# Optimization experiments

Measured on AMD Instinct MI355X. Metric: run time of the kernel, lower is better.

## Reference

```python
import jax, jax.numpy as jnp
import numpy as np


def setup_inputs() -> dict:
    key = jax.random.key(0)
    k1, k2, k3, k4, k5 = jax.random.split(key, 5)
    B, C, H, W = 8, 512, 128, 128
    C2 = 128  # key_dim
    x = jax.random.normal(k1, (B, C, H, W), dtype=jnp.float32)
    # 1x1 conv weights stored as [out_ch, in_ch] (kernel is 1x1)
    wq = jax.random.normal(k2, (C2, C), dtype=jnp.float32) * (1.0 / np.sqrt(C))
    bq = jax.random.normal(k3, (C2,), dtype=jnp.float32) * 0.01
    wk = jax.random.normal(k4, (C2, C), dtype=jnp.float32) * (1.0 / np.sqrt(C))
    bk = jax.random.normal(k5, (C2,), dtype=jnp.float32) * 0.01
    return {"x": x, "wq": wq, "bq": bq, "wk": wk, "bk": bk}


def reference(x, wq, bq, wk, bk):
    # x: [B, C, H, W]
    # 1x1 conv projections (query_conv / key_conv)
    q = jnp.einsum('bchw,kc->bkhw', x, wq) + bq[None, :, None, None]  # [B,C2,H,W]
    k = jnp.einsum('bchw,kc->bkhw', x, wk) + bk[None, :, None, None]  # [B,C2,H,W]

    # --- attention along H axis (batched over W) ---
    # query_h = key.permute(0,3,2,1): [B,W,H,C2]; key_h = query.permute(0,3,1,2): [B,W,C2,H]
    energy_h = jnp.einsum('bwhc,bcgw->bwhg', jnp.transpose(k, (0, 3, 2, 1)), q)  # [B,W,H,H]
    attn_h = jax.nn.softmax(energy_h, axis=-1)
    # value_h = x.permute(0,3,2,1): [B,W,H,C]; out: [B,W,H,C] -> permute(0,3,2,1) -> [B,C,H,W]
    out_h = jnp.einsum('bwhg,bcgw->bchw', attn_h, x)

    # --- attention along W axis (batched over H) ---
    # query_w = key.permute(0,2,3,1): [B,H,W,C2]; key_w = query.permute(0,2,1,3): [B,H,C2,W]
    energy_w = jnp.einsum('bhwc,bchv->bhwv', jnp.transpose(k, (0, 2, 3, 1)), q)  # [B,H,W,W]
    attn_w = jax.nn.softmax(energy_w, axis=-1)
    # value_w = x.permute(0,2,3,1): [B,H,W,C]; out: [B,H,W,C] -> permute(0,3,1,2) -> [B,C,H,W]
    out_w = jnp.einsum('bhwv,bchv->bchw', attn_w, x)

    return out_h + out_w
```

## Files before the change

kernel.cpp:

```cpp
#include <hip/hip_runtime.h>
#include <hip/hip_fp16.h>

#define NB 8
#define NC 512
#define NK 128
#define NP 128
#define NHW 16384

typedef unsigned short u16;
typedef unsigned int u32;
typedef float f32x4 __attribute__((ext_vector_type(4)));
typedef _Float16 f16x8 __attribute__((ext_vector_type(8)));

__device__ __forceinline__ u16 f2h(float f) { return __half_as_ushort(__float2half(f)); }
__device__ __forceinline__ float h2f(u16 u) { return __half2float(__ushort_as_half(u)); }

__global__ __launch_bounds__(256) void wconv_kernel(const float* __restrict__ wq,
                                                    const float* __restrict__ wk,
                                                    u16* __restrict__ wh) {
    int row = blockIdx.x;
    const float* src = (row < 128) ? (wq + (size_t)row * NC) : (wk + (size_t)(row - 128) * NC);
    int t = threadIdx.x;
    float2 v = *(const float2*)(src + t * 2);
    ushort2 o; o.x = f2h(v.x); o.y = f2h(v.y);
    *(ushort2*)(wh + (size_t)row * NC + t * 2) = o;
}

__global__ __launch_bounds__(256) void convtr_kernel(const float* __restrict__ x,
                                                     u16* __restrict__ xt) {
    __shared__ u16 ts[32][36];
    int plane = blockIdx.y;
    int tile  = blockIdx.x;
    int h0 = (tile >> 2) * 32, w0 = (tile & 3) * 32;
    const float* ip = x + (size_t)plane * NHW;
    u16* op = xt + (size_t)plane * NHW;
    int r  = threadIdx.x >> 3;
    int c4 = (threadIdx.x & 7) * 4;
    float4 v = *(const float4*)(ip + (h0 + r) * NP + w0 + c4);
    ts[r][c4 + 0] = f2h(v.x); ts[r][c4 + 1] = f2h(v.y);
    ts[r][c4 + 2] = f2h(v.z); ts[r][c4 + 3] = f2h(v.w);
    __syncthreads();
    ushort4 o;
    o.x = ts[c4 + 0][r]; o.y = ts[c4 + 1][r]; o.z = ts[c4 + 2][r]; o.w = ts[c4 + 3][r];
    *(ushort4*)(op + (w0 + r) * NP + h0 + c4) = o;
}

#define XROW 40
__device__ __forceinline__ int xt2_off(int p, int cw) {
    int sw = ((p >> 3) & 3) << 2;
    return p * XROW + 2 * (cw ^ sw);
}

__global__ __launch_bounds__(256, 3) void proj_kernel(const float* __restrict__ x,
                                                      const u16* __restrict__ wh,
                                                      const float* __restrict__ bq,
                                                      const float* __restrict__ bk,
                                                      u16* __restrict__ q,
                                                      u16* __restrict__ k) {
    __shared__ __align__(16) u16 smem[9216];
    int b  = blockIdx.y;
    int p0 = blockIdx.x * 64;
    int tid = threadIdx.x;
    int lane = tid & 63, w = tid >> 6;
    int ln = lane & 15, g = lane >> 4;

    float biasv[4];
#pragma unroll
    for (int nf = 0; nf < 4; nf++) {
        int oc = w * 64 + nf * 16 + ln;
        biasv[nf] = (oc < 128) ? bq[oc] : bk[oc - 128];
    }

    f32x4 acc[4][4];
#pragma unroll
    for (int mf = 0; mf < 4; mf++)
#pragma unroll
        for (int nf = 0; nf < 4; nf++) acc[mf][nf] = 0.0f;

    int si  = tid >> 4;
    int spx = (tid & 15) * 4;

#define STAGE(buf, c0)                                                                  \
    {                                                                                   \
        const float* xa = x + ((size_t)(b * NC + (c0) + 2 * si)) * NHW + p0 + spx;      \
        const float* xb = xa + NHW;                                                     \
        float4 a0 = *(const float4*)xa;                                                 \
        float4 b0 = *(const float4*)xb;                                                 \
        float av[4] = {a0.x, a0.y, a0.z, a0.w};                                         \
        float bv[4] = {b0.x, b0.y, b0.z, b0.w};                                         \
        _Pragma("unroll") for (int j = 0; j < 4; j++) {                                 \
            ushort2 pk;                                                                 \
            pk.x = f2h(av[j]); pk.y = f2h(bv[j]);                                       \
            *(ushort2*)&smem[(buf) * 2560 + xt2_off(spx + j, si)] = pk;                 \
        }                                                                               \
    }

    STAGE(0, 0);
    __syncthreads();
    for (int t = 0; t < 16; ++t) {
        int c0 = t * 32;
        if (t < 15) STAGE((t + 1) & 1, c0 + 32);
        f16x8 bf[4];
#pragma unroll
        for (int nf = 0; nf < 4; nf++)
            bf[nf] = *(const f16x8*)&wh[((size_t)(w * 64 + nf * 16 + ln)) * NC + c0 + g * 8];
        f16x8 af[4];
#pragma unroll
        for (int mf = 0; mf < 4; mf++)
            af[mf] = *(const f16x8*)&smem[(t & 1) * 2560 + xt2_off(mf * 16 + ln, g * 4)];
#pragma unroll
        for (int mf = 0; mf < 4; mf++)
#pragma unroll
            for (int nf = 0; nf < 4; nf++)
                acc[mf][nf] = __builtin_amdgcn_mfma_f32_16x16x32_f16(af[mf], bf[nf], acc[mf][nf], 0, 0, 0);
        __syncthreads();
    }
#undef STAGE

#pragma unroll
    for (int pass = 0; pass < 2; pass++) {
        if ((w >> 1) == pass) {
            int colbase = (w & 1) * 64;
#pragma unroll
            for (int mf = 0; mf < 4; mf++)
#pragma unroll
                for (int nf = 0; nf < 4; nf++)
#pragma unroll
                    for (int rg = 0; rg < 4; rg++) {
                        int p = mf * 16 + g * 4 + rg;
                        smem[p * 136 + colbase + nf * 16 + ln] = f2h(acc[mf][nf][rg] + biasv[nf]);
                    }
        }
        __syncthreads();
        {
            int p = tid >> 2, seg = tid & 3;
            u16* dst = (pass == 0 ? q : k) + ((size_t)(b * NHW + p0 + p)) * NK + seg * 32;
            const u16* srcl = &smem[p * 136 + seg * 32];
            *(uint4*)(dst)     = *(const uint4*)(srcl);
            *(uint4*)(dst + 8) = *(const uint4*)(srcl + 8);
            *(uint4*)(dst + 16) = *(const uint4*)(srcl + 16);
            *(uint4*)(dst + 24) = *(const uint4*)(srcl + 24);
        }
        __syncthreads();
    }
}

template <int TR>
__global__ __launch_bounds__(256) void attn_kernel(const u16* __restrict__ q,
                                                   const u16* __restrict__ k,
                                                   const void* __restrict__ vsrc,
                                                   void* __restrict__ osrc) {
    __shared__ __align__(16) u16 smem[2 * 128 * 136];
    __shared__ float redmax[256];
    __shared__ float redsum[256];
    u16* Ks = smem;
    u16* Qs = smem + 128 * 136;
    u16* Al = smem;
    u16* Vl = smem + 128 * 136;

    int r = blockIdx.x, b = blockIdx.y;
    int tid = threadIdx.x;
    int lane = tid & 63, w = tid >> 6;
    int ln = lane & 15, g = lane >> 4;

    const size_t base = TR ? ((size_t)b * NHW + r) * NK : ((size_t)b * NHW + (size_t)r * NP) * NK;
    const int qrs = TR ? NP * NK : NK;

    {
        int j = tid >> 1, hf = tid & 1;
        const u16* qp2 = q + base + (size_t)j * qrs + hf * 64;
        const u16* kp2 = k + base + (size_t)j * qrs + hf * 64;
#pragma unroll
        for (int e = 0; e < 8; e++) {
            *(uint4*)&Qs[j * 136 + hf * 64 + e * 8] = *(const uint4*)(qp2 + e * 8);
            *(uint4*)&Ks[j * 136 + hf * 64 + e * 8] = *(const uint4*)(kp2 + e * 8);
        }
    }
    __syncthreads();

    int wj = w >> 1, wi = w & 1;
    f32x4 e[4][4];
#pragma unroll
    for (int mf = 0; mf < 4; mf++)
#pragma unroll
        for (int nf = 0; nf < 4; nf++) e[mf][nf] = 0.0f;
#pragma unroll
    for (int ks = 0; ks < 4; ks++) {
        f16x8 qa[4], kb[4];
#pragma unroll
        for (int mf = 0; mf < 4; mf++)
            qa[mf] = *(const f16x8*)&Qs[(wj * 64 + mf * 16 + ln) * 136 + ks * 32 + g * 8];
#pragma unroll
        for (int nf = 0; nf < 4; nf++)
            kb[nf] = *(const f16x8*)&Ks[(wi * 64 + nf * 16 + ln) * 136 + ks * 32 + g * 8];
#pragma unroll
        for (int mf = 0; mf < 4; mf++)
#pragma unroll
            for (int nf = 0; nf < 4; nf++)
                e[mf][nf] = __builtin_amdgcn_mfma_f32_16x16x32_f16(qa[mf], kb[nf], e[mf][nf], 0, 0, 0);
    }

    float pm[4];
#pragma unroll
    for (int nf = 0; nf < 4; nf++) {
        pm[nf] = -3.0e38f;
#pragma unroll
        for (int mf = 0; mf < 4; mf++)
#pragma unroll
            for (int rg = 0; rg < 4; rg++) pm[nf] = fmaxf(pm[nf], e[mf][nf][rg]);
        pm[nf] = fmaxf(pm[nf], __shfl_xor(pm[nf], 16));
        pm[nf] = fmaxf(pm[nf], __shfl_xor(pm[nf], 32));
    }
    if (g == 0) {
#pragma unroll
        for (int nf = 0; nf < 4; nf++) redmax[wj * 128 + wi * 64 + nf * 16 + ln] = pm[nf];
    }
    __syncthreads();
    float fm[4];
#pragma unroll
    for (int nf = 0; nf < 4; nf++) {
        int i = wi * 64 + nf * 16 + ln;
        fm[nf] = fmaxf(redmax[i], redmax[128 + i]);
    }
    float ps[4] = {0.f, 0.f, 0.f, 0.f};
#pragma unroll
    for (int mf = 0; mf < 4; mf++)
#pragma unroll
        for (int nf = 0; nf < 4; nf++)
#pragma unroll
            for (int rg = 0; rg < 4; rg++) {
                float v = __expf(e[mf][nf][rg] - fm[nf]);
                e[mf][nf][rg] = v;
                ps[nf] += v;
            }
#pragma unroll
    for (int nf = 0; nf < 4; nf++) {
        ps[nf] += __shfl_xor(ps[nf], 16);
        ps[nf] += __shfl_xor(ps[nf], 32);
    }
    if (g == 0) {
#pragma unroll
        for (int nf = 0; nf < 4; nf++) redsum[wj * 128 + wi * 64 + nf * 16 + ln] = ps[nf];
    }
    __syncthreads();
    float ivs[4];
#pragma unroll
    for (int nf = 0; nf < 4; nf++) {
        int i = wi * 64 + nf * 16 + ln;
        ivs[nf] = 1.0f / (redsum[i] + redsum[128 + i]);
    }
#pragma unroll
    for (int mf = 0; mf < 4; mf++)
#pragma unroll
        for (int nf = 0; nf < 4; nf++) {
            ushort4 pk;
            pk.x = f2h(e[mf][nf][0] * ivs[nf]);
            pk.y = f2h(e[mf][nf][1] * ivs[nf]);
            pk.z = f2h(e[mf][nf][2] * ivs[nf]);
            pk.w = f2h(e[mf][nf][3] * ivs[nf]);
            *(ushort4*)&Al[(wi * 64 + nf * 16 + ln) * 136 + wj * 64 + mf * 16 + g * 4] = pk;
        }
    __syncthreads();

    int wc = w >> 1, wi2 = w & 1;
    f16x8 bfr[4][4];
#pragma unroll
    for (int nf2 = 0; nf2 < 4; nf2++)
#pragma unroll
        for (int js = 0; js < 4; js++)
            bfr[nf2][js] = *(const f16x8*)&Al[(wi2 * 64 + nf2 * 16 + ln) * 136 + js * 32 + g * 8];

    for (int c0 = 0; c0 < NC; c0 += 64) {
        {
            int cc = tid >> 2, ch = (tid & 3) * 32;
            if (TR == 0) {
                const float* vp = (const float*)vsrc + ((size_t)(b * NC + c0 + cc)) * NHW + (size_t)r * NP + ch;
                u16 tmp[32];
#pragma unroll
                for (int q4 = 0; q4 < 8; q4++) {
                    float4 vv = *(const float4*)(vp + q4 * 4);
                    tmp[q4 * 4 + 0] = f2h(vv.x);
                    tmp[q4 * 4 + 1] = f2h(vv.y);
                    tmp[q4 * 4 + 2] = f2h(vv.z);
                    tmp[q4 * 4 + 3] = f2h(vv.w);
                }
#pragma unroll
                for (int q8 = 0; q8 < 4; q8++)
                    *(uint4*)&Vl[cc * 136 + ch + q8 * 8] = *(uint4*)&tmp[q8 * 8];
            } else {
                const u16* vp = (const u16*)vsrc + ((size_t)(b * NC + c0 + cc)) * NHW + (size_t)r * NP + ch;
#pragma unroll
                for (int q8 = 0; q8 < 4; q8++)
                    *(uint4*)&Vl[cc * 136 + ch + q8 * 8] = *(const uint4*)(vp + q8 * 8);
            }
        }
        __syncthreads();
        f32x4 o[2][4];
#pragma unroll
        for (int mf2 = 0; mf2 < 2; mf2++)
#pragma unroll
            for (int nf2 = 0; nf2 < 4; nf2++) o[mf2][nf2] = 0.0f;
#pragma unroll
        for (int js = 0; js < 4; js++) {
            f16x8 va[2];
#pragma unroll
            for (int mf2 = 0; mf2 < 2; mf2++)
                va[mf2] = *(const f16x8*)&Vl[(wc * 32 + mf2 * 16 + ln) * 136 + js * 32 + g * 8];
#pragma unroll
            for (int mf2 = 0; mf2 < 2; mf2++)
#pragma unroll
                for (int nf2 = 0; nf2 < 4; nf2++)
                    o[mf2][nf2] = __builtin_amdgcn_mfma_f32_16x16x32_f16(va[mf2], bfr[nf2][js], o[mf2][nf2], 0, 0, 0);
        }
#pragma unroll
        for (int mf2 = 0; mf2 < 2; mf2++)
#pragma unroll
            for (int nf2 = 0; nf2 < 4; nf2++)
#pragma unroll
                for (int rg = 0; rg < 4; rg++) {
                    int ci = c0 + wc * 32 + mf2 * 16 + g * 4 + rg;
                    int ii = wi2 * 64 + nf2 * 16 + ln;
                    size_t oa = ((size_t)(b * NC + ci)) * NHW + (size_t)r * NP + ii;
                    if (TR == 0) ((float*)osrc)[oa] = o[mf2][nf2][rg];
                    else         ((u16*)osrc)[oa] = f2h(o[mf2][nf2][rg]);
                }
        __syncthreads();
    }
}

__global__ __launch_bounds__(256) void addtr_kernel(const u16* __restrict__ oht,
                                                    float* __restrict__ out) {
    __shared__ u16 ts[32][36];
    int plane = blockIdx.y;
    int tile  = blockIdx.x;
    int h0 = (tile >> 2) * 32, w0 = (tile & 3) * 32;
    int r  = threadIdx.x >> 3;
    int c4 = (threadIdx.x & 7) * 4;
    ushort4 v = *(const ushort4*)(oht + (size_t)plane * NHW + (w0 + r) * NP + h0 + c4);
    ts[r][c4 + 0] = v.x; ts[r][c4 + 1] = v.y; ts[r][c4 + 2] = v.z; ts[r][c4 + 3] = v.w;
    __syncthreads();
    float* dst = out + (size_t)plane * NHW + (h0 + r) * NP + w0 + c4;
    float4 cur = *(const float4*)dst;
    cur.x += h2f(ts[c4 + 0][r]);
    cur.y += h2f(ts[c4 + 1][r]);
    cur.z += h2f(ts[c4 + 2][r]);
    cur.w += h2f(ts[c4 + 3][r]);
    *(float4*)dst = cur;
}

extern "C" void kernel_launch(void* const* d_in, const int* in_sizes, int n_in,
                              void* d_out, int out_size, void* d_ws, size_t ws_size,
                              hipStream_t stream) {
    const float* x  = (const float*)d_in[0];
    const float* wq = (const float*)d_in[1];
    const float* bq = (const float*)d_in[2];
    const float* wk = (const float*)d_in[3];
    const float* bk = (const float*)d_in[4];
    float* out = (float*)d_out;

    const size_t QKE = (size_t)NB * NHW * NK;
    const size_t XE  = (size_t)NB * NC * NHW;
    u16* q   = (u16*)d_ws;
    u16* k   = q + QKE;
    u16* xt  = k + QKE;
    u16* oht = xt + XE;
    u16* wh  = oht + XE;

    dim3 blk(256);

    wconv_kernel<<<dim3(256), blk, 0, stream>>>(wq, wk, wh);
    convtr_kernel<<<dim3(16, NB * NC), blk, 0, stream>>>(x, xt);
    proj_kernel<<<dim3(NHW / 64, NB), blk, 0, stream>>>(x, wh, bq, bk, q, k);
    attn_kernel<1><<<dim3(NP, NB), blk, 0, stream>>>(q, k, (const void*)xt, (void*)oht);
    attn_kernel<0><<<dim3(NP, NB), blk, 0, stream>>>(q, k, (const void*)x, (void*)out);
    addtr_kernel<<<dim3(16, NB * NC), blk, 0, stream>>>(oht, out);
}
```

Before: 505.2 us.

## Prefetch next V chunk into registers and store W-attention output as fp16

The attention kernel now loads the next 64-channel V slice into registers while MFMAs run on the current slice, overlapping global loads with compute. When the workspace is large enough, the W-axis attention writes fp16 output to a scratch buffer and a new combine kernel reads both fp16 partial outputs and writes the fp32 result. This avoids an fp32 write followed by a read-modify-write of the output. It adds register pressure from the prefetch buffer and lowers the precision of the W-branch output to fp16.

Result: faster. 494.8 us (-2.1%).

```diff
diff --git a/kernel.cpp b/kernel.cpp
--- a/kernel.cpp
+++ b/kernel.cpp
@@ -145,7 +145,7 @@
     }
 }
 
-template <int TR>
+template <int TR, int OH>
 __global__ __launch_bounds__(256) void attn_kernel(const u16* __restrict__ q,
                                                    const u16* __restrict__ k,
                                                    const void* __restrict__ vsrc,
@@ -270,31 +270,33 @@
         for (int js = 0; js < 4; js++)
             bfr[nf2][js] = *(const f16x8*)&Al[(wi2 * 64 + nf2 * 16 + ln) * 136 + js * 32 + g * 8];
 
+    int cc = tid >> 2, ch = (tid & 3) * 32;
+    u16 vh[32];
+#define LOADV(c0)                                                                           \
+    {                                                                                       \
+        if (TR == 0) {                                                                      \
+            const float* vn = (const float*)vsrc + ((size_t)(b * NC + (c0) + cc)) * NHW +   \
+                              (size_t)r * NP + ch;                                          \
+            _Pragma("unroll") for (int e2 = 0; e2 < 8; e2++) {                              \
+                float4 vv = *(const float4*)(vn + e2 * 4);                                  \
+                vh[e2 * 4 + 0] = f2h(vv.x); vh[e2 * 4 + 1] = f2h(vv.y);                     \
+                vh[e2 * 4 + 2] = f2h(vv.z); vh[e2 * 4 + 3] = f2h(vv.w);                     \
+            }                                                                               \
+        } else {                                                                            \
+            const u16* vn = (const u16*)vsrc + ((size_t)(b * NC + (c0) + cc)) * NHW +       \
+                            (size_t)r * NP + ch;                                            \
+            _Pragma("unroll") for (int e2 = 0; e2 < 4; e2++)                                \
+                *(uint4*)&vh[e2 * 8] = *(const uint4*)(vn + e2 * 8);                        \
+        }                                                                                   \
+    }
+
+    LOADV(0);
     for (int c0 = 0; c0 < NC; c0 += 64) {
-        {
-            int cc = tid >> 2, ch = (tid & 3) * 32;
-            if (TR == 0) {
-                const float* vp = (const float*)vsrc + ((size_t)(b * NC + c0 + cc)) * NHW + (size_t)r * NP + ch;
-                u16 tmp[32];
-#pragma unroll
-                for (int q4 = 0; q4 < 8; q4++) {
-                    float4 vv = *(const float4*)(vp + q4 * 4);
-                    tmp[q4 * 4 + 0] = f2h(vv.x);
-                    tmp[q4 * 4 + 1] = f2h(vv.y);
-                    tmp[q4 * 4 + 2] = f2h(vv.z);
-                    tmp[q4 * 4 + 3] = f2h(vv.w);
-                }
-#pragma unroll
-                for (int q8 = 0; q8 < 4; q8++)
-                    *(uint4*)&Vl[cc * 136 + ch + q8 * 8] = *(uint4*)&tmp[q8 * 8];
-            } else {
-                const u16* vp = (const u16*)vsrc + ((size_t)(b * NC + c0 + cc)) * NHW + (size_t)r * NP + ch;
-#pragma unroll
-                for (int q8 = 0; q8 < 4; q8++)
-                    *(uint4*)&Vl[cc * 136 + ch + q8 * 8] = *(const uint4*)(vp + q8 * 8);
-            }
-        }
+#pragma unroll
+        for (int e2 = 0; e2 < 4; e2++)
+            *(uint4*)&Vl[cc * 136 + ch + e2 * 8] = *(uint4*)&vh[e2 * 8];
         __syncthreads();
+        if (c0 + 64 < NC) LOADV(c0 + 64);
         f32x4 o[2][4];
 #pragma unroll
         for (int mf2 = 0; mf2 < 2; mf2++)
@@ -321,11 +323,33 @@
                     int ci = c0 + wc * 32 + mf2 * 16 + g * 4 + rg;
                     int ii = wi2 * 64 + nf2 * 16 + ln;
                     size_t oa = ((size_t)(b * NC + ci)) * NHW + (size_t)r * NP + ii;
-                    if (TR == 0) ((float*)osrc)[oa] = o[mf2][nf2][rg];
-                    else         ((u16*)osrc)[oa] = f2h(o[mf2][nf2][rg]);
+                    if (OH) ((u16*)osrc)[oa] = f2h(o[mf2][nf2][rg]);
+                    else    ((float*)osrc)[oa] = o[mf2][nf2][rg];
                 }
         __syncthreads();
     }
+#undef LOADV
+}
+
+__global__ __launch_bounds__(256) void combine_kernel(const u16* __restrict__ owh,
+                                                      const u16* __restrict__ oht,
+                                                      float* __restrict__ out) {
+    __shared__ u16 ts[32][36];
+    int plane = blockIdx.y;
+    int tile  = blockIdx.x;
+    int h0 = (tile >> 2) * 32, w0 = (tile & 3) * 32;
+    int r  = threadIdx.x >> 3;
+    int c4 = (threadIdx.x & 7) * 4;
+    ushort4 v = *(const ushort4*)(oht + (size_t)plane * NHW + (w0 + r) * NP + h0 + c4);
+    ts[r][c4 + 0] = v.x; ts[r][c4 + 1] = v.y; ts[r][c4 + 2] = v.z; ts[r][c4 + 3] = v.w;
+    __syncthreads();
+    ushort4 a = *(const ushort4*)(owh + (size_t)plane * NHW + (h0 + r) * NP + w0 + c4);
+    float4 o;
+    o.x = h2f(a.x) + h2f(ts[c4 + 0][r]);
+    o.y = h2f(a.y) + h2f(ts[c4 + 1][r]);
+    o.z = h2f(a.z) + h2f(ts[c4 + 2][r]);
+    o.w = h2f(a.w) + h2f(ts[c4 + 3][r]);
+    *(float4*)(out + (size_t)plane * NHW + (h0 + r) * NP + w0 + c4) = o;
 }
 
 __global__ __launch_bounds__(256) void addtr_kernel(const u16* __restrict__ oht,
@@ -360,18 +384,27 @@
 
     const size_t QKE = (size_t)NB * NHW * NK;
     const size_t XE  = (size_t)NB * NC * NHW;
-    u16* q   = (u16*)d_ws;
+    const size_t WHE = (size_t)256 * 512;
+    u16* wh  = (u16*)d_ws;
+    u16* q   = wh + WHE;
     u16* k   = q + QKE;
     u16* xt  = k + QKE;
     u16* oht = xt + XE;
-    u16* wh  = oht + XE;
+    u16* owh = oht + XE;
+    const size_t need_big = (WHE + 2 * QKE + 3 * XE) * sizeof(u16);
+    const bool big = ws_size >= need_big;
 
     dim3 blk(256);
 
     wconv_kernel<<<dim3(256), blk, 0, stream>>>(wq, wk, wh);
     convtr_kernel<<<dim3(16, NB * NC), blk, 0, stream>>>(x, xt);
     proj_kernel<<<dim3(NHW / 64, NB), blk, 0, stream>>>(x, wh, bq, bk, q, k);
-    attn_kernel<1><<<dim3(NP, NB), blk, 0, stream>>>(q, k, (const void*)xt, (void*)oht);
-    attn_kernel<0><<<dim3(NP, NB), blk, 0, stream>>>(q, k, (const void*)x, (void*)out);
-    addtr_kernel<<<dim3(16, NB * NC), blk, 0, stream>>>(oht, out);
-}
+    attn_kernel<1, 1><<<dim3(NP, NB), blk, 0, stream>>>(q, k, (const void*)xt, (void*)oht);
+    if (big) {
+        attn_kernel<0, 1><<<dim3(NP, NB), blk, 0, stream>>>(q, k, (const void*)x, (void*)owh);
+        combine_kernel<<<dim3(16, NB * NC), blk, 0, stream>>>(owh, oht, out);
+    } else {
+        attn_kernel<0, 0><<<dim3(NP, NB), blk, 0, stream>>>(q, k, (const void*)x, (void*)out);
+        addtr_kernel<<<dim3(16, NB * NC), blk, 0, stream>>>(oht, out);
+    }
+}
```
